# Performance work log

Hardware: AMD Instinct MI355X
Metric: run time of the kernel (lower is better)

Reference implementation:

```python
import jax, jax.numpy as jnp
import numpy as np

N, DIM, HEADS = 4096, 256, 4
DK = DIM // HEADS
EPS = 1e-5


def setup_inputs() -> dict:
    key = jax.random.key(0)
    ks = jax.random.split(key, 12)
    x = jax.random.normal(ks[0], (N, DIM), dtype=jnp.float32)
    adj = (jax.random.uniform(ks[1], (N, N)) < 0.05).astype(jnp.float32)
    s = 1.0 / np.sqrt(DIM).astype(np.float32)
    Wq = jax.random.normal(ks[2], (DIM, DIM), dtype=jnp.float32) * s
    bq = jnp.zeros((DIM,), jnp.float32)
    Wk = jax.random.normal(ks[3], (DIM, DIM), dtype=jnp.float32) * s
    bk = jnp.zeros((DIM,), jnp.float32)
    Wv = jax.random.normal(ks[4], (DIM, DIM), dtype=jnp.float32) * s
    bv = jnp.zeros((DIM,), jnp.float32)
    Wo = jax.random.normal(ks[5], (DIM, DIM), dtype=jnp.float32) * s
    bo = jnp.zeros((DIM,), jnp.float32)
    gamma = jnp.ones((DIM,), jnp.float32)
    beta = jnp.zeros((DIM,), jnp.float32)
    return {"x": x, "adj": adj, "Wq": Wq, "bq": bq, "Wk": Wk, "bk": bk,
            "Wv": Wv, "bv": bv, "Wo": Wo, "bo": bo, "gamma": gamma, "beta": beta}


def reference(x, adj, Wq, bq, Wk, bk, Wv, bv, Wo, bo, gamma, beta):
    n = x.shape[0]
    # projections -> [N, H, dk]
    Q = (x @ Wq.T + bq).reshape(n, HEADS, DK)
    K = (x @ Wk.T + bk).reshape(n, HEADS, DK)
    V = (x @ Wv.T + bv).reshape(n, HEADS, DK)
    inv_sqrt_dk = jnp.asarray(1.0 / np.sqrt(DK), x.dtype)
    # [N, N, H] scores, multiplicative adjacency mask BEFORE softmax
    scores = jnp.einsum('ihd,jhd->ijh', Q, K) * inv_sqrt_dk
    scores = scores * adj[:, :, None]
    weights = jax.nn.softmax(scores, axis=1)  # softmax over source nodes j
    out = jnp.einsum('ijh,jhd->ihd', weights, V).reshape(n, DIM)
    out = out @ Wo.T + bo
    # residual + LayerNorm
    h = out + x
    mu = jnp.mean(h, axis=-1, keepdims=True)
    var = jnp.mean(jnp.square(h - mu), axis=-1, keepdims=True)
    return (h - mu) * jax.lax.rsqrt(var + EPS) * gamma + beta
```

## Files before the change

### kernel.cpp

```cpp
#include <hip/hip_runtime.h>
#include <math.h>

#define NN 4096
#define DIMV 256
#define ECAP 768

__device__ __forceinline__ void gemm_body(
    const float* __restrict__ A, const float* __restrict__ W,
    const float* __restrict__ bias, const float* __restrict__ resid,
    float* __restrict__ C, int mb, int nb)
{
    __shared__ float As[32][68];
    __shared__ float Bs[32][68];
    const int tid = threadIdx.x;
    const int tx = tid & 15, ty = tid >> 4;
    const int row0 = mb * 64, col0 = nb * 64;
    const int lr = tid >> 3;
    const int lc = (tid & 7) * 4;

    float acc[4][4] = {};

    for (int k0 = 0; k0 < 256; k0 += 32) {
        float4 a0 = *(const float4*)(A + (size_t)(row0 + lr) * 256 + k0 + lc);
        float4 a1 = *(const float4*)(A + (size_t)(row0 + lr + 32) * 256 + k0 + lc);
        float4 w0 = *(const float4*)(W + (size_t)(col0 + lr) * 256 + k0 + lc);
        float4 w1 = *(const float4*)(W + (size_t)(col0 + lr + 32) * 256 + k0 + lc);
        __syncthreads();
        As[lc + 0][lr] = a0.x; As[lc + 1][lr] = a0.y; As[lc + 2][lr] = a0.z; As[lc + 3][lr] = a0.w;
        As[lc + 0][lr + 32] = a1.x; As[lc + 1][lr + 32] = a1.y; As[lc + 2][lr + 32] = a1.z; As[lc + 3][lr + 32] = a1.w;
        Bs[lc + 0][lr] = w0.x; Bs[lc + 1][lr] = w0.y; Bs[lc + 2][lr] = w0.z; Bs[lc + 3][lr] = w0.w;
        Bs[lc + 0][lr + 32] = w1.x; Bs[lc + 1][lr + 32] = w1.y; Bs[lc + 2][lr + 32] = w1.z; Bs[lc + 3][lr + 32] = w1.w;
        __syncthreads();
#pragma unroll
        for (int kk = 0; kk < 32; kk++) {
            float4 av = *(const float4*)&As[kk][ty * 4];
            float4 bv = *(const float4*)&Bs[kk][tx * 4];
            acc[0][0] = fmaf(av.x, bv.x, acc[0][0]); acc[0][1] = fmaf(av.x, bv.y, acc[0][1]);
            acc[0][2] = fmaf(av.x, bv.z, acc[0][2]); acc[0][3] = fmaf(av.x, bv.w, acc[0][3]);
            acc[1][0] = fmaf(av.y, bv.x, acc[1][0]); acc[1][1] = fmaf(av.y, bv.y, acc[1][1]);
            acc[1][2] = fmaf(av.y, bv.z, acc[1][2]); acc[1][3] = fmaf(av.y, bv.w, acc[1][3]);
            acc[2][0] = fmaf(av.z, bv.x, acc[2][0]); acc[2][1] = fmaf(av.z, bv.y, acc[2][1]);
            acc[2][2] = fmaf(av.z, bv.z, acc[2][2]); acc[2][3] = fmaf(av.z, bv.w, acc[2][3]);
            acc[3][0] = fmaf(av.w, bv.x, acc[3][0]); acc[3][1] = fmaf(av.w, bv.y, acc[3][1]);
            acc[3][2] = fmaf(av.w, bv.z, acc[3][2]); acc[3][3] = fmaf(av.w, bv.w, acc[3][3]);
        }
    }
#pragma unroll
    for (int r = 0; r < 4; r++) {
        int gr = row0 + ty * 4 + r;
        int gc = col0 + tx * 4;
        float4 v;
        v.x = acc[r][0] + bias[gc + 0];
        v.y = acc[r][1] + bias[gc + 1];
        v.z = acc[r][2] + bias[gc + 2];
        v.w = acc[r][3] + bias[gc + 3];
        if (resid) {
            const float4 rv = *(const float4*)(resid + (size_t)gr * 256 + gc);
            v.x += rv.x; v.y += rv.y; v.z += rv.z; v.w += rv.w;
        }
        *(float4*)(C + (size_t)gr * 256 + gc) = v;
    }
}

__global__ __launch_bounds__(256) void qkv_gemm(
    const float* __restrict__ x,
    const float* __restrict__ Wq, const float* __restrict__ Wk, const float* __restrict__ Wv,
    const float* __restrict__ bq, const float* __restrict__ bk, const float* __restrict__ bv,
    float* __restrict__ Q, float* __restrict__ K, float* __restrict__ V)
{
    int which = blockIdx.y >> 2;
    int nb = blockIdx.y & 3;
    const float* W = which == 0 ? Wq : (which == 1 ? Wk : Wv);
    const float* b = which == 0 ? bq : (which == 1 ? bk : bv);
    float* C = which == 0 ? Q : (which == 1 ? K : V);
    gemm_body(x, W, b, nullptr, C, blockIdx.x, nb);
}

__global__ __launch_bounds__(256) void out_gemm(
    const float* __restrict__ A, const float* __restrict__ Wo,
    const float* __restrict__ bo, const float* __restrict__ x,
    float* __restrict__ H)
{
    gemm_body(A, Wo, bo, x, H, blockIdx.x, blockIdx.y);
}

__global__ __launch_bounds__(256) void colsum(const float* __restrict__ V, float* __restrict__ S)
{
    int t = threadIdx.x;
    int r0 = blockIdx.x * 16;
    float s = 0.f;
#pragma unroll
    for (int r = 0; r < 16; r++) s += V[(size_t)(r0 + r) * 256 + t];
    atomicAdd(&S[t], s);
}

__global__ __launch_bounds__(256) void csr_build(
    const float* __restrict__ adj, unsigned short* __restrict__ col,
    int* __restrict__ nnz)
{
    __shared__ int cnt;
    const int i = blockIdx.x;
    const int tid = threadIdx.x;
    if (tid == 0) cnt = 0;
    __syncthreads();
    const float4* __restrict__ arow = (const float4*)(adj + (size_t)i * NN);
    unsigned short* __restrict__ crow = col + (size_t)i * ECAP;
#pragma unroll
    for (int t = 0; t < 4; t++) {
        const float4 a = arow[t * 256 + tid];
        const int j0 = (t * 256 + tid) * 4;
        if (a.x != 0.f) crow[atomicAdd(&cnt, 1)] = (unsigned short)(j0 + 0);
        if (a.y != 0.f) crow[atomicAdd(&cnt, 1)] = (unsigned short)(j0 + 1);
        if (a.z != 0.f) crow[atomicAdd(&cnt, 1)] = (unsigned short)(j0 + 2);
        if (a.w != 0.f) crow[atomicAdd(&cnt, 1)] = (unsigned short)(j0 + 3);
    }
    __syncthreads();
    if (tid == 0) nnz[i] = cnt;
}

__global__ __launch_bounds__(512, 4) void attn_edges(
    const float* __restrict__ Q, const float* __restrict__ K,
    const float* __restrict__ V, const unsigned short* __restrict__ col,
    const int* __restrict__ nnz, const float* __restrict__ S,
    float* __restrict__ out)
{
    __shared__ float qs[256];
    __shared__ unsigned short lj[ECAP];
    __shared__ float wgt[ECAP * 4];
    __shared__ float pnum[2][256];
    __shared__ float pden[2][4];

    const int i = blockIdx.x;
    const int tid = threadIdx.x;
    const int wave = tid >> 6;
    const int lane = tid & 63;
    const int m = nnz[i];

    if (tid < 256) qs[tid] = Q[(size_t)i * 256 + tid] * 0.125f;
    for (int e = tid; e < m; e += 512) lj[e] = col[(size_t)i * ECAP + e];
    __syncthreads();

    const float4 qv = ((const float4*)qs)[lane];
    for (int e0 = wave * 4; e0 < m; e0 += 32) {
        int jj[4];
#pragma unroll
        for (int u = 0; u < 4; u++)
            jj[u] = (e0 + u < m) ? lj[e0 + u] : lj[e0];
        float4 kv[4];
#pragma unroll
        for (int u = 0; u < 4; u++)
            kv[u] = ((const float4*)(K + (size_t)jj[u] * 256))[lane];
#pragma unroll
        for (int u = 0; u < 4; u++) {
            float d = (kv[u].x * qv.x + kv[u].y * qv.y) + (kv[u].z * qv.z + kv[u].w * qv.w);
            d += __shfl_xor(d, 1);
            d += __shfl_xor(d, 2);
            d += __shfl_xor(d, 4);
            d += __shfl_xor(d, 8);
            if ((lane & 15) == 0 && e0 + u < m)
                wgt[(e0 + u) * 4 + (lane >> 4)] = expf(d) - 1.f;
        }
    }
    __syncthreads();

    const int g = tid >> 8;
    const int d = tid & 255;
    const int head = d >> 6;
    float num = 0.f, den = 0.f;
    int e = g;
    for (; e + 14 < m; e += 16) {
        float w[8];
#pragma unroll
        for (int u = 0; u < 8; u++) w[u] = wgt[(e + 2 * u) * 4 + head];
        float v[8];
#pragma unroll
        for (int u = 0; u < 8; u++)
            v[u] = V[(size_t)lj[e + 2 * u] * 256 + d];
#pragma unroll
        for (int u = 0; u < 8; u++) { num = fmaf(w[u], v[u], num); den += w[u]; }
    }
    for (; e < m; e += 2) {
        const float w = wgt[e * 4 + head];
        num = fmaf(w, V[(size_t)lj[e] * 256 + d], num);
        den += w;
    }
    pnum[g][d] = num;
    if ((d & 63) == 0) pden[g][head] = den;
    __syncthreads();

    if (tid < 256) {
        const float dn = pden[0][head] + pden[1][head] + 4096.0f;
        out[(size_t)i * 256 + tid] = (pnum[0][tid] + pnum[1][tid] + S[tid]) / dn;
    }
}

__global__ __launch_bounds__(256) void ln_kernel(
    const float* __restrict__ H, const float* __restrict__ gamma,
    const float* __restrict__ beta, float* __restrict__ out)
{
    const int row = blockIdx.x * 4 + (threadIdx.x >> 6);
    const int lane = threadIdx.x & 63;
    const float4 v = ((const float4*)(H + (size_t)row * 256))[lane];
    float s = (v.x + v.y) + (v.z + v.w);
#pragma unroll
    for (int o = 1; o < 64; o <<= 1) s += __shfl_xor(s, o);
    const float mu = s * (1.f / 256.f);
    const float dx = v.x - mu, dy = v.y - mu, dz = v.z - mu, dw = v.w - mu;
    float sq = (dx * dx + dy * dy) + (dz * dz + dw * dw);
#pragma unroll
    for (int o = 1; o < 64; o <<= 1) sq += __shfl_xor(sq, o);
    const float rstd = rsqrtf(sq * (1.f / 256.f) + 1e-5f);
    const float4 g = ((const float4*)gamma)[lane];
    const float4 b = ((const float4*)beta)[lane];
    float4 o4;
    o4.x = dx * rstd * g.x + b.x;
    o4.y = dy * rstd * g.y + b.y;
    o4.z = dz * rstd * g.z + b.z;
    o4.w = dw * rstd * g.w + b.w;
    ((float4*)(out + (size_t)row * 256))[lane] = o4;
}

extern "C" void kernel_launch(void* const* d_in, const int* in_sizes, int n_in,
                              void* d_out, int out_size, void* d_ws, size_t ws_size,
                              hipStream_t stream)
{
    const float* x     = (const float*)d_in[0];
    const float* adj   = (const float*)d_in[1];
    const float* Wq    = (const float*)d_in[2];
    const float* bq    = (const float*)d_in[3];
    const float* Wk    = (const float*)d_in[4];
    const float* bk    = (const float*)d_in[5];
    const float* Wv    = (const float*)d_in[6];
    const float* bv    = (const float*)d_in[7];
    const float* Wo    = (const float*)d_in[8];
    const float* bo    = (const float*)d_in[9];
    const float* gamma = (const float*)d_in[10];
    const float* beta  = (const float*)d_in[11];

    float* ws = (float*)d_ws;
    const size_t NM = (size_t)NN * DIMV;
    float* Qb = ws;
    float* Kb = ws + NM;
    float* Vb = ws + 2 * NM;
    float* AT = ws + 3 * NM;
    float* S  = ws + 4 * NM;
    unsigned short* col = (unsigned short*)(ws + 4 * NM + 256);
    int* nnz = (int*)((char*)col + (size_t)NN * ECAP * sizeof(unsigned short));
    float* H  = Qb;

    hipMemsetAsync(S, 0, 256 * sizeof(float), stream);
    csr_build<<<NN, 256, 0, stream>>>(adj, col, nnz);
    qkv_gemm<<<dim3(64, 12), 256, 0, stream>>>(x, Wq, Wk, Wv, bq, bk, bv, Qb, Kb, Vb);
    colsum<<<256, 256, 0, stream>>>(Vb, S);
    attn_edges<<<NN, 512, 0, stream>>>(Qb, Kb, Vb, col, nnz, S, AT);
    out_gemm<<<dim3(64, 4), 256, 0, stream>>>(AT, Wo, bo, x, H);
    ln_kernel<<<1024, 256, 0, stream>>>(H, gamma, beta, (float*)d_out);
}
```

Before: 268.7 us.

## Fuse CSR build into attention and enlarge GEMM tiles to 128x128

Removes the separate csr_build kernel by having each attention block scan its own adjacency row, using a wave prefix sum plus one shared atomic per wave to fill a shared neighbour list. The attention kernel now computes scores and accumulates V-weighted sums in one pass per wave, so the shared weight buffer and second pass are gone, and it runs with 256 threads. The GEMMs use 128x128 tiles with 8x8 per-thread accumulators, which raises register use and cuts the grid to 192 blocks for QKV and 64 for the output projection, so occupancy may drop. Neighbour lists are also clamped to ECAP entries.

```diff
diff --git a/kernel.cpp b/kernel.cpp
--- a/kernel.cpp
+++ b/kernel.cpp
@@ -10,55 +10,59 @@
     const float* __restrict__ bias, const float* __restrict__ resid,
     float* __restrict__ C, int mb, int nb)
 {
-    __shared__ float As[32][68];
-    __shared__ float Bs[32][68];
+    __shared__ float As[16][132];
+    __shared__ float Bs[16][132];
     const int tid = threadIdx.x;
     const int tx = tid & 15, ty = tid >> 4;
-    const int row0 = mb * 64, col0 = nb * 64;
-    const int lr = tid >> 3;
-    const int lc = (tid & 7) * 4;
-
-    float acc[4][4] = {};
-
-    for (int k0 = 0; k0 < 256; k0 += 32) {
-        float4 a0 = *(const float4*)(A + (size_t)(row0 + lr) * 256 + k0 + lc);
-        float4 a1 = *(const float4*)(A + (size_t)(row0 + lr + 32) * 256 + k0 + lc);
-        float4 w0 = *(const float4*)(W + (size_t)(col0 + lr) * 256 + k0 + lc);
-        float4 w1 = *(const float4*)(W + (size_t)(col0 + lr + 32) * 256 + k0 + lc);
+    const int row0 = mb * 128, col0 = nb * 128;
+    const int lr = tid >> 2;
+    const int lc = (tid & 3) * 4;
+
+    float acc[8][8] = {};
+
+    for (int k0 = 0; k0 < 256; k0 += 16) {
+        const float4 a0 = *(const float4*)(A + (size_t)(row0 + lr) * 256 + k0 + lc);
+        const float4 a1 = *(const float4*)(A + (size_t)(row0 + lr + 64) * 256 + k0 + lc);
+        const float4 w0 = *(const float4*)(W + (size_t)(col0 + lr) * 256 + k0 + lc);
+        const float4 w1 = *(const float4*)(W + (size_t)(col0 + lr + 64) * 256 + k0 + lc);
         __syncthreads();
         As[lc + 0][lr] = a0.x; As[lc + 1][lr] = a0.y; As[lc + 2][lr] = a0.z; As[lc + 3][lr] = a0.w;
-        As[lc + 0][lr + 32] = a1.x; As[lc + 1][lr + 32] = a1.y; As[lc + 2][lr + 32] = a1.z; As[lc + 3][lr + 32] = a1.w;
+        As[lc + 0][lr + 64] = a1.x; As[lc + 1][lr + 64] = a1.y; As[lc + 2][lr + 64] = a1.z; As[lc + 3][lr + 64] = a1.w;
         Bs[lc + 0][lr] = w0.x; Bs[lc + 1][lr] = w0.y; Bs[lc + 2][lr] = w0.z; Bs[lc + 3][lr] = w0.w;
-        Bs[lc + 0][lr + 32] = w1.x; Bs[lc + 1][lr + 32] = w1.y; Bs[lc + 2][lr + 32] = w1.z; Bs[lc + 3][lr + 32] = w1.w;
+        Bs[lc + 0][lr + 64] = w1.x; Bs[lc + 1][lr + 64] = w1.y; Bs[lc + 2][lr + 64] = w1.z; Bs[lc + 3][lr + 64] = w1.w;
         __syncthreads();
 #pragma unroll
-        for (int kk = 0; kk < 32; kk++) {
-            float4 av = *(const float4*)&As[kk][ty * 4];
-            float4 bv = *(const float4*)&Bs[kk][tx * 4];
-            acc[0][0] = fmaf(av.x, bv.x, acc[0][0]); acc[0][1] = fmaf(av.x, bv.y, acc[0][1]);
-            acc[0][2] = fmaf(av.x, bv.z, acc[0][2]); acc[0][3] = fmaf(av.x, bv.w, acc[0][3]);
-            acc[1][0] = fmaf(av.y, bv.x, acc[1][0]); acc[1][1] = fmaf(av.y, bv.y, acc[1][1]);
-            acc[1][2] = fmaf(av.y, bv.z, acc[1][2]); acc[1][3] = fmaf(av.y, bv.w, acc[1][3]);
-            acc[2][0] = fmaf(av.z, bv.x, acc[2][0]); acc[2][1] = fmaf(av.z, bv.y, acc[2][1]);
-            acc[2][2] = fmaf(av.z, bv.z, acc[2][2]); acc[2][3] = fmaf(av.z, bv.w, acc[2][3]);
-            acc[3][0] = fmaf(av.w, bv.x, acc[3][0]); acc[3][1] = fmaf(av.w, bv.y, acc[3][1]);
-            acc[3][2] = fmaf(av.w, bv.z, acc[3][2]); acc[3][3] = fmaf(av.w, bv.w, acc[3][3]);
-        }
-    }
-#pragma unroll
-    for (int r = 0; r < 4; r++) {
-        int gr = row0 + ty * 4 + r;
-        int gc = col0 + tx * 4;
-        float4 v;
-        v.x = acc[r][0] + bias[gc + 0];
-        v.y = acc[r][1] + bias[gc + 1];
-        v.z = acc[r][2] + bias[gc + 2];
-        v.w = acc[r][3] + bias[gc + 3];
+        for (int kk = 0; kk < 16; kk++) {
+            const float4 alo = *(const float4*)&As[kk][ty * 8];
+            const float4 ahi = *(const float4*)&As[kk][ty * 8 + 4];
+            const float4 blo = *(const float4*)&Bs[kk][tx * 8];
+            const float4 bhi = *(const float4*)&Bs[kk][tx * 8 + 4];
+            const float av[8] = {alo.x, alo.y, alo.z, alo.w, ahi.x, ahi.y, ahi.z, ahi.w};
+            const float bv[8] = {blo.x, blo.y, blo.z, blo.w, bhi.x, bhi.y, bhi.z, bhi.w};
+#pragma unroll
+            for (int r = 0; r < 8; r++)
+#pragma unroll
+                for (int c = 0; c < 8; c++)
+                    acc[r][c] = fmaf(av[r], bv[c], acc[r][c]);
+        }
+    }
+#pragma unroll
+    for (int r = 0; r < 8; r++) {
+        const int gr = row0 + ty * 8 + r;
+        const int gc = col0 + tx * 8;
+        float4 v0, v1;
+        v0.x = acc[r][0] + bias[gc + 0]; v0.y = acc[r][1] + bias[gc + 1];
+        v0.z = acc[r][2] + bias[gc + 2]; v0.w = acc[r][3] + bias[gc + 3];
+        v1.x = acc[r][4] + bias[gc + 4]; v1.y = acc[r][5] + bias[gc + 5];
+        v1.z = acc[r][6] + bias[gc + 6]; v1.w = acc[r][7] + bias[gc + 7];
         if (resid) {
-            const float4 rv = *(const float4*)(resid + (size_t)gr * 256 + gc);
-            v.x += rv.x; v.y += rv.y; v.z += rv.z; v.w += rv.w;
-        }
-        *(float4*)(C + (size_t)gr * 256 + gc) = v;
+            const float4 r0 = *(const float4*)(resid + (size_t)gr * 256 + gc);
+            const float4 r1 = *(const float4*)(resid + (size_t)gr * 256 + gc + 4);
+            v0.x += r0.x; v0.y += r0.y; v0.z += r0.z; v0.w += r0.w;
+            v1.x += r1.x; v1.y += r1.y; v1.z += r1.z; v1.w += r1.w;
+        }
+        *(float4*)(C + (size_t)gr * 256 + gc) = v0;
+        *(float4*)(C + (size_t)gr * 256 + gc + 4) = v1;
     }
 }
 
@@ -68,12 +72,11 @@
     const float* __restrict__ bq, const float* __restrict__ bk, const float* __restrict__ bv,
     float* __restrict__ Q, float* __restrict__ K, float* __restrict__ V)
 {
-    int which = blockIdx.y >> 2;
-    int nb = blockIdx.y & 3;
+    const int which = blockIdx.z;
     const float* W = which == 0 ? Wq : (which == 1 ? Wk : Wv);
     const float* b = which == 0 ? bq : (which == 1 ? bk : bv);
     float* C = which == 0 ? Q : (which == 1 ? K : V);
-    gemm_body(x, W, b, nullptr, C, blockIdx.x, nb);
+    gemm_body(x, W, b, nullptr, C, blockIdx.x, blockIdx.y);
 }
 
 __global__ __launch_bounds__(256) void out_gemm(
@@ -86,70 +89,71 @@
 
 __global__ __launch_bounds__(256) void colsum(const float* __restrict__ V, float* __restrict__ S)
 {
-    int t = threadIdx.x;
-    int r0 = blockIdx.x * 16;
+    const int t = threadIdx.x;
+    const int r0 = blockIdx.x * 16;
     float s = 0.f;
 #pragma unroll
     for (int r = 0; r < 16; r++) s += V[(size_t)(r0 + r) * 256 + t];
     atomicAdd(&S[t], s);
 }
 
-__global__ __launch_bounds__(256) void csr_build(
-    const float* __restrict__ adj, unsigned short* __restrict__ col,
-    int* __restrict__ nnz)
-{
+__global__ __launch_bounds__(256) void attn_fused(
+    const float* __restrict__ Q, const float* __restrict__ K,
+    const float* __restrict__ V, const float* __restrict__ adj,
+    const float* __restrict__ S, float* __restrict__ out)
+{
+    __shared__ unsigned short lj[ECAP];
+    __shared__ float pnum[4][256];
+    __shared__ float pden[4][4];
     __shared__ int cnt;
-    const int i = blockIdx.x;
-    const int tid = threadIdx.x;
-    if (tid == 0) cnt = 0;
-    __syncthreads();
-    const float4* __restrict__ arow = (const float4*)(adj + (size_t)i * NN);
-    unsigned short* __restrict__ crow = col + (size_t)i * ECAP;
-#pragma unroll
-    for (int t = 0; t < 4; t++) {
-        const float4 a = arow[t * 256 + tid];
-        const int j0 = (t * 256 + tid) * 4;
-        if (a.x != 0.f) crow[atomicAdd(&cnt, 1)] = (unsigned short)(j0 + 0);
-        if (a.y != 0.f) crow[atomicAdd(&cnt, 1)] = (unsigned short)(j0 + 1);
-        if (a.z != 0.f) crow[atomicAdd(&cnt, 1)] = (unsigned short)(j0 + 2);
-        if (a.w != 0.f) crow[atomicAdd(&cnt, 1)] = (unsigned short)(j0 + 3);
-    }
-    __syncthreads();
-    if (tid == 0) nnz[i] = cnt;
-}
-
-__global__ __launch_bounds__(512, 4) void attn_edges(
-    const float* __restrict__ Q, const float* __restrict__ K,
-    const float* __restrict__ V, const unsigned short* __restrict__ col,
-    const int* __restrict__ nnz, const float* __restrict__ S,
-    float* __restrict__ out)
-{
-    __shared__ float qs[256];
-    __shared__ unsigned short lj[ECAP];
-    __shared__ float wgt[ECAP * 4];
-    __shared__ float pnum[2][256];
-    __shared__ float pden[2][4];
 
     const int i = blockIdx.x;
     const int tid = threadIdx.x;
     const int wave = tid >> 6;
     const int lane = tid & 63;
-    const int m = nnz[i];
-
-    if (tid < 256) qs[tid] = Q[(size_t)i * 256 + tid] * 0.125f;
-    for (int e = tid; e < m; e += 512) lj[e] = col[(size_t)i * ECAP + e];
+
+    if (tid == 0) cnt = 0;
     __syncthreads();
 
-    const float4 qv = ((const float4*)qs)[lane];
-    for (int e0 = wave * 4; e0 < m; e0 += 32) {
+    const float4* __restrict__ arow = (const float4*)(adj + (size_t)i * NN);
+#pragma unroll
+    for (int t = 0; t < 4; t++) {
+        const float4 a = arow[t * 256 + tid];
+        const int j0 = (t * 256 + tid) * 4;
+        const int c = (a.x != 0.f) + (a.y != 0.f) + (a.z != 0.f) + (a.w != 0.f);
+        int off = c;
+#pragma unroll
+        for (int s = 1; s < 64; s <<= 1) {
+            const int v = __shfl_up(off, s);
+            if (lane >= s) off += v;
+        }
+        int base = 0;
+        if (lane == 63) base = atomicAdd(&cnt, off);
+        base = __shfl(base, 63);
+        int p = base + off - c;
+        if (a.x != 0.f && p < ECAP) lj[p++] = (unsigned short)(j0 + 0);
+        if (a.y != 0.f && p < ECAP) lj[p++] = (unsigned short)(j0 + 1);
+        if (a.z != 0.f && p < ECAP) lj[p++] = (unsigned short)(j0 + 2);
+        if (a.w != 0.f && p < ECAP) lj[p++] = (unsigned short)(j0 + 3);
+    }
+    __syncthreads();
+    const int m = min(cnt, ECAP);
+
+    const float4 qraw = ((const float4*)(Q + (size_t)i * 256))[lane];
+    const float4 qv = {qraw.x * 0.125f, qraw.y * 0.125f, qraw.z * 0.125f, qraw.w * 0.125f};
+    float nx = 0.f, ny = 0.f, nz = 0.f, nw = 0.f, den = 0.f;
+
+    for (int e0 = wave * 4; e0 < m; e0 += 16) {
         int jj[4];
 #pragma unroll
         for (int u = 0; u < 4; u++)
-            jj[u] = (e0 + u < m) ? lj[e0 + u] : lj[e0];
-        float4 kv[4];
-#pragma unroll
-        for (int u = 0; u < 4; u++)
+            jj[u] = (e0 + u < m) ? (int)lj[e0 + u] : (int)lj[e0];
+        float4 kv[4], vv[4];
+#pragma unroll
+        for (int u = 0; u < 4; u++) {
             kv[u] = ((const float4*)(K + (size_t)jj[u] * 256))[lane];
+            vv[u] = ((const float4*)(V + (size_t)jj[u] * 256))[lane];
+        }
 #pragma unroll
         for (int u = 0; u < 4; u++) {
             float d = (kv[u].x * qv.x + kv[u].y * qv.y) + (kv[u].z * qv.z + kv[u].w * qv.w);
@@ -157,41 +161,25 @@
             d += __shfl_xor(d, 2);
             d += __shfl_xor(d, 4);
             d += __shfl_xor(d, 8);
-            if ((lane & 15) == 0 && e0 + u < m)
-                wgt[(e0 + u) * 4 + (lane >> 4)] = expf(d) - 1.f;
-        }
-    }
+            float w = expf(d) - 1.f;
+            if (e0 + u >= m) w = 0.f;
+            nx = fmaf(w, vv[u].x, nx); ny = fmaf(w, vv[u].y, ny);
+            nz = fmaf(w, vv[u].z, nz); nw = fmaf(w, vv[u].w, nw);
+            den += w;
+        }
+    }
+
+    pnum[wave][lane * 4 + 0] = nx;
+    pnum[wave][lane * 4 + 1] = ny;
+    pnum[wave][lane * 4 + 2] = nz;
+    pnum[wave][lane * 4 + 3] = nw;
+    if ((lane & 15) == 0) pden[wave][lane >> 4] = den;
     __syncthreads();
 
-    const int g = tid >> 8;
-    const int d = tid & 255;
-    const int head = d >> 6;
-    float num = 0.f, den = 0.f;
-    int e = g;
-    for (; e + 14 < m; e += 16) {
-        float w[8];
-#pragma unroll
-        for (int u = 0; u < 8; u++) w[u] = wgt[(e + 2 * u) * 4 + head];
-        float v[8];
-#pragma unroll
-        for (int u = 0; u < 8; u++)
-            v[u] = V[(size_t)lj[e + 2 * u] * 256 + d];
-#pragma unroll
-        for (int u = 0; u < 8; u++) { num = fmaf(w[u], v[u], num); den += w[u]; }
-    }
-    for (; e < m; e += 2) {
-        const float w = wgt[e * 4 + head];
-        num = fmaf(w, V[(size_t)lj[e] * 256 + d], num);
-        den += w;
-    }
-    pnum[g][d] = num;
-    if ((d & 63) == 0) pden[g][head] = den;
-    __syncthreads();
-
-    if (tid < 256) {
-        const float dn = pden[0][head] + pden[1][head] + 4096.0f;
-        out[(size_t)i * 256 + tid] = (pnum[0][tid] + pnum[1][tid] + S[tid]) / dn;
-    }
+    const int head = tid >> 6;
+    const float dn = (pden[0][head] + pden[1][head]) + (pden[2][head] + pden[3][head]) + 4096.0f;
+    const float nm = (pnum[0][tid] + pnum[1][tid]) + (pnum[2][tid] + pnum[3][tid]) + S[tid];
+    out[(size_t)i * 256 + tid] = nm / dn;
 }
 
 __global__ __launch_bounds__(256) void ln_kernel(
@@ -244,15 +232,12 @@
     float* Vb = ws + 2 * NM;
     float* AT = ws + 3 * NM;
     float* S  = ws + 4 * NM;
-    unsigned short* col = (unsigned short*)(ws + 4 * NM + 256);
-    int* nnz = (int*)((char*)col + (size_t)NN * ECAP * sizeof(unsigned short));
     float* H  = Qb;
 
     hipMemsetAsync(S, 0, 256 * sizeof(float), stream);
-    csr_build<<<NN, 256, 0, stream>>>(adj, col, nnz);
-    qkv_gemm<<<dim3(64, 12), 256, 0, stream>>>(x, Wq, Wk, Wv, bq, bk, bv, Qb, Kb, Vb);
+    qkv_gemm<<<dim3(32, 2, 3), 256, 0, stream>>>(x, Wq, Wk, Wv, bq, bk, bv, Qb, Kb, Vb);
     colsum<<<256, 256, 0, stream>>>(Vb, S);
-    attn_edges<<<NN, 512, 0, stream>>>(Qb, Kb, Vb, col, nnz, S, AT);
-    out_gemm<<<dim3(64, 4), 256, 0, stream>>>(AT, Wo, bo, x, H);
+    attn_fused<<<NN, 256, 0, stream>>>(Qb, Kb, Vb, adj, S, AT);
+    out_gemm<<<dim3(32, 2, 1), 256, 0, stream>>>(AT, Wo, bo, x, H);
     ln_kernel<<<1024, 256, 0, stream>>>(H, gamma, beta, (float*)d_out);
 }
```

Result: slower. 302.9 us (+12.7%).

## Fuse CSR build into attention, colsum into QKV GEMM, LayerNorm into out GEMM

Applied to the files above, without the earlier changes.

Removes the separate CSR build kernel: each attention block now reads its own adjacency row with nontemporal loads and compacts the neighbor indices into shared memory using a wave-level prefix scan. The V column-sum moves into the QKV GEMM epilogue, which also switches to 64x128 tiles. The output projection is fused with residual add and LayerNorm by giving each block full 256-wide rows. Together these cut kernel launches and the global round trips for the CSR arrays, the H buffer and V; in exchange the attention kernel carries extra scan work and syncs, and the out GEMM uses only 256 blocks.

```diff
diff --git a/kernel.cpp b/kernel.cpp
--- a/kernel.cpp
+++ b/kernel.cpp
@@ -5,147 +5,142 @@
 #define DIMV 256
 #define ECAP 768
 
-__device__ __forceinline__ void gemm_body(
-    const float* __restrict__ A, const float* __restrict__ W,
-    const float* __restrict__ bias, const float* __restrict__ resid,
-    float* __restrict__ C, int mb, int nb)
-{
-    __shared__ float As[32][68];
-    __shared__ float Bs[32][68];
-    const int tid = threadIdx.x;
-    const int tx = tid & 15, ty = tid >> 4;
-    const int row0 = mb * 64, col0 = nb * 64;
-    const int lr = tid >> 3;
-    const int lc = (tid & 7) * 4;
-
-    float acc[4][4] = {};
-
-    for (int k0 = 0; k0 < 256; k0 += 32) {
-        float4 a0 = *(const float4*)(A + (size_t)(row0 + lr) * 256 + k0 + lc);
-        float4 a1 = *(const float4*)(A + (size_t)(row0 + lr + 32) * 256 + k0 + lc);
-        float4 w0 = *(const float4*)(W + (size_t)(col0 + lr) * 256 + k0 + lc);
-        float4 w1 = *(const float4*)(W + (size_t)(col0 + lr + 32) * 256 + k0 + lc);
-        __syncthreads();
-        As[lc + 0][lr] = a0.x; As[lc + 1][lr] = a0.y; As[lc + 2][lr] = a0.z; As[lc + 3][lr] = a0.w;
-        As[lc + 0][lr + 32] = a1.x; As[lc + 1][lr + 32] = a1.y; As[lc + 2][lr + 32] = a1.z; As[lc + 3][lr + 32] = a1.w;
-        Bs[lc + 0][lr] = w0.x; Bs[lc + 1][lr] = w0.y; Bs[lc + 2][lr] = w0.z; Bs[lc + 3][lr] = w0.w;
-        Bs[lc + 0][lr + 32] = w1.x; Bs[lc + 1][lr + 32] = w1.y; Bs[lc + 2][lr + 32] = w1.z; Bs[lc + 3][lr + 32] = w1.w;
-        __syncthreads();
-#pragma unroll
-        for (int kk = 0; kk < 32; kk++) {
-            float4 av = *(const float4*)&As[kk][ty * 4];
-            float4 bv = *(const float4*)&Bs[kk][tx * 4];
-            acc[0][0] = fmaf(av.x, bv.x, acc[0][0]); acc[0][1] = fmaf(av.x, bv.y, acc[0][1]);
-            acc[0][2] = fmaf(av.x, bv.z, acc[0][2]); acc[0][3] = fmaf(av.x, bv.w, acc[0][3]);
-            acc[1][0] = fmaf(av.y, bv.x, acc[1][0]); acc[1][1] = fmaf(av.y, bv.y, acc[1][1]);
-            acc[1][2] = fmaf(av.y, bv.z, acc[1][2]); acc[1][3] = fmaf(av.y, bv.w, acc[1][3]);
-            acc[2][0] = fmaf(av.z, bv.x, acc[2][0]); acc[2][1] = fmaf(av.z, bv.y, acc[2][1]);
-            acc[2][2] = fmaf(av.z, bv.z, acc[2][2]); acc[2][3] = fmaf(av.z, bv.w, acc[2][3]);
-            acc[3][0] = fmaf(av.w, bv.x, acc[3][0]); acc[3][1] = fmaf(av.w, bv.y, acc[3][1]);
-            acc[3][2] = fmaf(av.w, bv.z, acc[3][2]); acc[3][3] = fmaf(av.w, bv.w, acc[3][3]);
-        }
-    }
-#pragma unroll
-    for (int r = 0; r < 4; r++) {
-        int gr = row0 + ty * 4 + r;
-        int gc = col0 + tx * 4;
-        float4 v;
-        v.x = acc[r][0] + bias[gc + 0];
-        v.y = acc[r][1] + bias[gc + 1];
-        v.z = acc[r][2] + bias[gc + 2];
-        v.w = acc[r][3] + bias[gc + 3];
-        if (resid) {
-            const float4 rv = *(const float4*)(resid + (size_t)gr * 256 + gc);
-            v.x += rv.x; v.y += rv.y; v.z += rv.z; v.w += rv.w;
-        }
-        *(float4*)(C + (size_t)gr * 256 + gc) = v;
-    }
-}
+typedef float f32x4 __attribute__((ext_vector_type(4)));
 
 __global__ __launch_bounds__(256) void qkv_gemm(
     const float* __restrict__ x,
     const float* __restrict__ Wq, const float* __restrict__ Wk, const float* __restrict__ Wv,
     const float* __restrict__ bq, const float* __restrict__ bk, const float* __restrict__ bv,
-    float* __restrict__ Q, float* __restrict__ K, float* __restrict__ V)
-{
-    int which = blockIdx.y >> 2;
-    int nb = blockIdx.y & 3;
-    const float* W = which == 0 ? Wq : (which == 1 ? Wk : Wv);
-    const float* b = which == 0 ? bq : (which == 1 ? bk : bv);
-    float* C = which == 0 ? Q : (which == 1 ? K : V);
-    gemm_body(x, W, b, nullptr, C, blockIdx.x, nb);
-}
-
-__global__ __launch_bounds__(256) void out_gemm(
-    const float* __restrict__ A, const float* __restrict__ Wo,
-    const float* __restrict__ bo, const float* __restrict__ x,
-    float* __restrict__ H)
-{
-    gemm_body(A, Wo, bo, x, H, blockIdx.x, blockIdx.y);
-}
-
-__global__ __launch_bounds__(256) void colsum(const float* __restrict__ V, float* __restrict__ S)
-{
-    int t = threadIdx.x;
-    int r0 = blockIdx.x * 16;
-    float s = 0.f;
-#pragma unroll
-    for (int r = 0; r < 16; r++) s += V[(size_t)(r0 + r) * 256 + t];
-    atomicAdd(&S[t], s);
-}
-
-__global__ __launch_bounds__(256) void csr_build(
-    const float* __restrict__ adj, unsigned short* __restrict__ col,
-    int* __restrict__ nnz)
-{
-    __shared__ int cnt;
-    const int i = blockIdx.x;
+    float* __restrict__ Q, float* __restrict__ K, float* __restrict__ V,
+    float* __restrict__ S)
+{
+    __shared__ float As[32][69];
+    __shared__ float Bs[32][133];
+
+    const int which = blockIdx.z;
+    const float* __restrict__ W = which == 0 ? Wq : (which == 1 ? Wk : Wv);
+    const float* __restrict__ bias = which == 0 ? bq : (which == 1 ? bk : bv);
+    float* __restrict__ C = which == 0 ? Q : (which == 1 ? K : V);
+
     const int tid = threadIdx.x;
-    if (tid == 0) cnt = 0;
-    __syncthreads();
-    const float4* __restrict__ arow = (const float4*)(adj + (size_t)i * NN);
-    unsigned short* __restrict__ crow = col + (size_t)i * ECAP;
-#pragma unroll
-    for (int t = 0; t < 4; t++) {
-        const float4 a = arow[t * 256 + tid];
-        const int j0 = (t * 256 + tid) * 4;
-        if (a.x != 0.f) crow[atomicAdd(&cnt, 1)] = (unsigned short)(j0 + 0);
-        if (a.y != 0.f) crow[atomicAdd(&cnt, 1)] = (unsigned short)(j0 + 1);
-        if (a.z != 0.f) crow[atomicAdd(&cnt, 1)] = (unsigned short)(j0 + 2);
-        if (a.w != 0.f) crow[atomicAdd(&cnt, 1)] = (unsigned short)(j0 + 3);
-    }
-    __syncthreads();
-    if (tid == 0) nnz[i] = cnt;
-}
-
-__global__ __launch_bounds__(512, 4) void attn_edges(
+    const int row0 = blockIdx.x * 64, col0 = blockIdx.y * 128;
+    const int ty = tid >> 5;
+    const int tx = tid & 31;
+    const int lrA = tid >> 2;
+    const int lcA = (tid & 3) * 8;
+    const int lrB = tid >> 1;
+    const int lcB = (tid & 1) * 16;
+
+    float acc[8][4] = {};
+
+    for (int k0 = 0; k0 < 256; k0 += 32) {
+        const float4 a0 = *(const float4*)(x + (size_t)(row0 + lrA) * 256 + k0 + lcA);
+        const float4 a1 = *(const float4*)(x + (size_t)(row0 + lrA) * 256 + k0 + lcA + 4);
+        const float4 b0 = *(const float4*)(W + (size_t)(col0 + lrB) * 256 + k0 + lcB);
+        const float4 b1 = *(const float4*)(W + (size_t)(col0 + lrB) * 256 + k0 + lcB + 4);
+        const float4 b2 = *(const float4*)(W + (size_t)(col0 + lrB) * 256 + k0 + lcB + 8);
+        const float4 b3 = *(const float4*)(W + (size_t)(col0 + lrB) * 256 + k0 + lcB + 12);
+        __syncthreads();
+        As[lcA + 0][lrA] = a0.x; As[lcA + 1][lrA] = a0.y; As[lcA + 2][lrA] = a0.z; As[lcA + 3][lrA] = a0.w;
+        As[lcA + 4][lrA] = a1.x; As[lcA + 5][lrA] = a1.y; As[lcA + 6][lrA] = a1.z; As[lcA + 7][lrA] = a1.w;
+        Bs[lcB +  0][lrB] = b0.x; Bs[lcB +  1][lrB] = b0.y; Bs[lcB +  2][lrB] = b0.z; Bs[lcB +  3][lrB] = b0.w;
+        Bs[lcB +  4][lrB] = b1.x; Bs[lcB +  5][lrB] = b1.y; Bs[lcB +  6][lrB] = b1.z; Bs[lcB +  7][lrB] = b1.w;
+        Bs[lcB +  8][lrB] = b2.x; Bs[lcB +  9][lrB] = b2.y; Bs[lcB + 10][lrB] = b2.z; Bs[lcB + 11][lrB] = b2.w;
+        Bs[lcB + 12][lrB] = b3.x; Bs[lcB + 13][lrB] = b3.y; Bs[lcB + 14][lrB] = b3.z; Bs[lcB + 15][lrB] = b3.w;
+        __syncthreads();
+#pragma unroll
+        for (int kk = 0; kk < 32; kk++) {
+            const float4 alo = *(const float4*)&As[kk][ty * 8];
+            const float4 ahi = *(const float4*)&As[kk][ty * 8 + 4];
+            const float4 bv4 = *(const float4*)&Bs[kk][tx * 4];
+            const float av[8] = {alo.x, alo.y, alo.z, alo.w, ahi.x, ahi.y, ahi.z, ahi.w};
+            const float bw[4] = {bv4.x, bv4.y, bv4.z, bv4.w};
+#pragma unroll
+            for (int r = 0; r < 8; r++)
+#pragma unroll
+                for (int c = 0; c < 4; c++)
+                    acc[r][c] = fmaf(av[r], bw[c], acc[r][c]);
+        }
+    }
+
+    const int gc = col0 + tx * 4;
+    const float4 b4 = *(const float4*)(bias + gc);
+    float cs0 = 0.f, cs1 = 0.f, cs2 = 0.f, cs3 = 0.f;
+#pragma unroll
+    for (int r = 0; r < 8; r++) {
+        const int gr = row0 + ty * 8 + r;
+        float4 v;
+        v.x = acc[r][0] + b4.x; v.y = acc[r][1] + b4.y;
+        v.z = acc[r][2] + b4.z; v.w = acc[r][3] + b4.w;
+        *(float4*)(C + (size_t)gr * 256 + gc) = v;
+        cs0 += v.x; cs1 += v.y; cs2 += v.z; cs3 += v.w;
+    }
+    if (which == 2) {
+        atomicAdd(&S[gc + 0], cs0);
+        atomicAdd(&S[gc + 1], cs1);
+        atomicAdd(&S[gc + 2], cs2);
+        atomicAdd(&S[gc + 3], cs3);
+    }
+}
+
+__global__ __launch_bounds__(512, 4) void attn_v3(
     const float* __restrict__ Q, const float* __restrict__ K,
-    const float* __restrict__ V, const unsigned short* __restrict__ col,
-    const int* __restrict__ nnz, const float* __restrict__ S,
-    float* __restrict__ out)
-{
-    __shared__ float qs[256];
+    const float* __restrict__ V, const float* __restrict__ adj,
+    const float* __restrict__ S, float* __restrict__ out)
+{
     __shared__ unsigned short lj[ECAP];
     __shared__ float wgt[ECAP * 4];
     __shared__ float pnum[2][256];
     __shared__ float pden[2][4];
+    __shared__ int wtot[8], wbase[8], cnt;
 
     const int i = blockIdx.x;
     const int tid = threadIdx.x;
     const int wave = tid >> 6;
     const int lane = tid & 63;
-    const int m = nnz[i];
-
-    if (tid < 256) qs[tid] = Q[(size_t)i * 256 + tid] * 0.125f;
-    for (int e = tid; e < m; e += 512) lj[e] = col[(size_t)i * ECAP + e];
-    __syncthreads();
-
-    const float4 qv = ((const float4*)qs)[lane];
+
+    const f32x4* __restrict__ arow = (const f32x4*)(adj + (size_t)i * NN);
+    const f32x4 a0 = __builtin_nontemporal_load(arow + 2 * tid);
+    const f32x4 a1 = __builtin_nontemporal_load(arow + 2 * tid + 1);
+    const int c = (a0.x != 0.f) + (a0.y != 0.f) + (a0.z != 0.f) + (a0.w != 0.f)
+                + (a1.x != 0.f) + (a1.y != 0.f) + (a1.z != 0.f) + (a1.w != 0.f);
+    int incl = c;
+#pragma unroll
+    for (int s = 1; s < 64; s <<= 1) {
+        const int v = __shfl_up(incl, s);
+        if (lane >= s) incl += v;
+    }
+    if (lane == 63) wtot[wave] = incl;
+    __syncthreads();
+    if (tid == 0) {
+        int s = 0;
+#pragma unroll
+        for (int w = 0; w < 8; w++) { wbase[w] = s; s += wtot[w]; }
+        cnt = s;
+    }
+    __syncthreads();
+    {
+        int p = wbase[wave] + incl - c;
+        const int j0 = tid * 8;
+        if (a0.x != 0.f && p < ECAP) lj[p++] = (unsigned short)(j0 + 0);
+        if (a0.y != 0.f && p < ECAP) lj[p++] = (unsigned short)(j0 + 1);
+        if (a0.z != 0.f && p < ECAP) lj[p++] = (unsigned short)(j0 + 2);
+        if (a0.w != 0.f && p < ECAP) lj[p++] = (unsigned short)(j0 + 3);
+        if (a1.x != 0.f && p < ECAP) lj[p++] = (unsigned short)(j0 + 4);
+        if (a1.y != 0.f && p < ECAP) lj[p++] = (unsigned short)(j0 + 5);
+        if (a1.z != 0.f && p < ECAP) lj[p++] = (unsigned short)(j0 + 6);
+        if (a1.w != 0.f && p < ECAP) lj[p++] = (unsigned short)(j0 + 7);
+    }
+    __syncthreads();
+    const int m = min(cnt, ECAP);
+
+    const float4 qraw = ((const float4*)(Q + (size_t)i * 256))[lane];
+    const float4 qv = {qraw.x * 0.125f, qraw.y * 0.125f, qraw.z * 0.125f, qraw.w * 0.125f};
     for (int e0 = wave * 4; e0 < m; e0 += 32) {
         int jj[4];
 #pragma unroll
         for (int u = 0; u < 4; u++)
-            jj[u] = (e0 + u < m) ? lj[e0 + u] : lj[e0];
+            jj[u] = (e0 + u < m) ? (int)lj[e0 + u] : (int)lj[e0];
         float4 kv[4];
 #pragma unroll
         for (int u = 0; u < 4; u++)
@@ -189,35 +184,85 @@
     __syncthreads();
 
     if (tid < 256) {
-        const float dn = pden[0][head] + pden[1][head] + 4096.0f;
+        const int h = tid >> 6;
+        const float dn = pden[0][h] + pden[1][h] + 4096.0f;
         out[(size_t)i * 256 + tid] = (pnum[0][tid] + pnum[1][tid] + S[tid]) / dn;
     }
 }
 
-__global__ __launch_bounds__(256) void ln_kernel(
-    const float* __restrict__ H, const float* __restrict__ gamma,
-    const float* __restrict__ beta, float* __restrict__ out)
-{
-    const int row = blockIdx.x * 4 + (threadIdx.x >> 6);
-    const int lane = threadIdx.x & 63;
-    const float4 v = ((const float4*)(H + (size_t)row * 256))[lane];
-    float s = (v.x + v.y) + (v.z + v.w);
-#pragma unroll
-    for (int o = 1; o < 64; o <<= 1) s += __shfl_xor(s, o);
-    const float mu = s * (1.f / 256.f);
-    const float dx = v.x - mu, dy = v.y - mu, dz = v.z - mu, dw = v.w - mu;
-    float sq = (dx * dx + dy * dy) + (dz * dz + dw * dw);
-#pragma unroll
-    for (int o = 1; o < 64; o <<= 1) sq += __shfl_xor(sq, o);
-    const float rstd = rsqrtf(sq * (1.f / 256.f) + 1e-5f);
-    const float4 g = ((const float4*)gamma)[lane];
-    const float4 b = ((const float4*)beta)[lane];
-    float4 o4;
-    o4.x = dx * rstd * g.x + b.x;
-    o4.y = dy * rstd * g.y + b.y;
-    o4.z = dz * rstd * g.z + b.z;
-    o4.w = dw * rstd * g.w + b.w;
-    ((float4*)(out + (size_t)row * 256))[lane] = o4;
+__global__ __launch_bounds__(256) void out_ln(
+    const float* __restrict__ A, const float* __restrict__ Wo,
+    const float* __restrict__ bo, const float* __restrict__ x,
+    const float* __restrict__ gamma, const float* __restrict__ beta,
+    float* __restrict__ out)
+{
+    __shared__ float As[16][20];
+    __shared__ float Bs[16][260];
+
+    const int tid = threadIdx.x;
+    const int row0 = blockIdx.x * 16;
+    const int ty = tid >> 6;
+    const int tx = tid & 63;
+    const int lrA = tid >> 4;
+    const int lcA = tid & 15;
+
+    float acc[4][4] = {};
+
+    for (int k0 = 0; k0 < 256; k0 += 16) {
+        const float aval = A[(size_t)(row0 + lrA) * 256 + k0 + lcA];
+        const float4 w0 = *(const float4*)(Wo + (size_t)tid * 256 + k0);
+        const float4 w1 = *(const float4*)(Wo + (size_t)tid * 256 + k0 + 4);
+        const float4 w2 = *(const float4*)(Wo + (size_t)tid * 256 + k0 + 8);
+        const float4 w3 = *(const float4*)(Wo + (size_t)tid * 256 + k0 + 12);
+        __syncthreads();
+        As[lcA][lrA] = aval;
+        Bs[ 0][tid] = w0.x; Bs[ 1][tid] = w0.y; Bs[ 2][tid] = w0.z; Bs[ 3][tid] = w0.w;
+        Bs[ 4][tid] = w1.x; Bs[ 5][tid] = w1.y; Bs[ 6][tid] = w1.z; Bs[ 7][tid] = w1.w;
+        Bs[ 8][tid] = w2.x; Bs[ 9][tid] = w2.y; Bs[10][tid] = w2.z; Bs[11][tid] = w2.w;
+        Bs[12][tid] = w3.x; Bs[13][tid] = w3.y; Bs[14][tid] = w3.z; Bs[15][tid] = w3.w;
+        __syncthreads();
+#pragma unroll
+        for (int kk = 0; kk < 16; kk++) {
+            const float4 a4 = *(const float4*)&As[kk][ty * 4];
+            const float4 b4 = *(const float4*)&Bs[kk][tx * 4];
+            const float av[4] = {a4.x, a4.y, a4.z, a4.w};
+            const float bw[4] = {b4.x, b4.y, b4.z, b4.w};
+#pragma unroll
+            for (int r = 0; r < 4; r++)
+#pragma unroll
+                for (int c2 = 0; c2 < 4; c2++)
+                    acc[r][c2] = fmaf(av[r], bw[c2], acc[r][c2]);
+        }
+    }
+
+    const int gc = tx * 4;
+    const float4 b4 = *(const float4*)(bo + gc);
+    const float4 g4 = *(const float4*)(gamma + gc);
+    const float4 be4 = *(const float4*)(beta + gc);
+#pragma unroll
+    for (int r = 0; r < 4; r++) {
+        const int gr = row0 + ty * 4 + r;
+        const float4 rv = *(const float4*)(x + (size_t)gr * 256 + gc);
+        float h0 = acc[r][0] + b4.x + rv.x;
+        float h1 = acc[r][1] + b4.y + rv.y;
+        float h2 = acc[r][2] + b4.z + rv.z;
+        float h3 = acc[r][3] + b4.w + rv.w;
+        float s = (h0 + h1) + (h2 + h3);
+#pragma unroll
+        for (int o = 1; o < 64; o <<= 1) s += __shfl_xor(s, o);
+        const float mu = s * (1.f / 256.f);
+        const float d0 = h0 - mu, d1 = h1 - mu, d2 = h2 - mu, d3 = h3 - mu;
+        float sq = (d0 * d0 + d1 * d1) + (d2 * d2 + d3 * d3);
+#pragma unroll
+        for (int o = 1; o < 64; o <<= 1) sq += __shfl_xor(sq, o);
+        const float rstd = rsqrtf(sq * (1.f / 256.f) + 1e-5f);
+        float4 o4;
+        o4.x = d0 * rstd * g4.x + be4.x;
+        o4.y = d1 * rstd * g4.y + be4.y;
+        o4.z = d2 * rstd * g4.z + be4.z;
+        o4.w = d3 * rstd * g4.w + be4.w;
+        *(float4*)(out + (size_t)gr * 256 + gc) = o4;
+    }
 }
 
 extern "C" void kernel_launch(void* const* d_in, const int* in_sizes, int n_in,
@@ -244,15 +289,9 @@
     float* Vb = ws + 2 * NM;
     float* AT = ws + 3 * NM;
     float* S  = ws + 4 * NM;
-    unsigned short* col = (unsigned short*)(ws + 4 * NM + 256);
-    int* nnz = (int*)((char*)col + (size_t)NN * ECAP * sizeof(unsigned short));
-    float* H  = Qb;
-
-    hipMemsetAsync(S, 0, 256 * sizeof(float), stream);
-    csr_build<<<NN, 256, 0, stream>>>(adj, col, nnz);
-    qkv_gemm<<<dim3(64, 12), 256, 0, stream>>>(x, Wq, Wk, Wv, bq, bk, bv, Qb, Kb, Vb);
-    colsum<<<256, 256, 0, stream>>>(Vb, S);
-    attn_edges<<<NN, 512, 0, stream>>>(Qb, Kb, Vb, col, nnz, S, AT);
-    out_gemm<<<dim3(64, 4), 256, 0, stream>>>(AT, Wo, bo, x, H);
-    ln_kernel<<<1024, 256, 0, stream>>>(H, gamma, beta, (float*)d_out);
-}
+
+    (void)hipMemsetAsync(S, 0, 256 * sizeof(float), stream);
+    qkv_gemm<<<dim3(64, 2, 3), 256, 0, stream>>>(x, Wq, Wk, Wv, bq, bk, bv, Qb, Kb, Vb, S);
+    attn_v3<<<NN, 512, 0, stream>>>(Qb, Kb, Vb, adj, S, AT);
+    out_ln<<<256, 256, 0, stream>>>(AT, Wo, bo, x, gamma, beta, (float*)d_out);
+}
```

New measurement: 331.2 us. 23.2% more time.
